# Kernel optimization log

Hardware: AMD Instinct MI355X
Metric: run time of the kernel (lower is better)

The kernel has to match this reference:

```python
import jax, jax.numpy as jnp
import numpy as np

BS = 16; N_PER = 1024; N = BS * N_PER; K = 9; E = N * K
H = 128; NODE_D = 64; EDGE_D = 16; RBF_DIM = 20; R_CUT = 1.0; L = 4; SF = 0.1


def setup_inputs():
    ks = jax.random.split(jax.random.key(0), 24)
    X = jax.random.normal(ks[0], (N, 3), dtype=jnp.float32) * 0.5
    node_attr = jax.random.normal(ks[1], (N, NODE_D), dtype=jnp.float32)
    edge_attr = jax.random.normal(ks[2], (E, EDGE_D), dtype=jnp.float32)
    idx = jnp.arange(N, dtype=jnp.int32)
    bid = idx // N_PER
    Seg = ((idx % N_PER) >= (N_PER // 2)).astype(jnp.int32)
    row = jnp.repeat(idx, K)
    col = (row // N_PER) * N_PER + jax.random.randint(ks[3], (E,), 0, N_PER, dtype=jnp.int32)
    edges = jnp.stack([row, col])

    def g(k, shape, fan):
        return jax.random.normal(k, shape, dtype=jnp.float32) * (1.0 / float(np.sqrt(fan)))

    MI = 2 * H + RBF_DIM + EDGE_D  # message MLP input dim
    return {
        'X': X, 'node_attr': node_attr, 'edge_attr': edge_attr,
        'W_in1': g(ks[4], (NODE_D, H), NODE_D), 'b_in1': jnp.zeros((H,), jnp.float32),
        'W_in2': g(ks[5], (H, H), H), 'b_in2': jnp.zeros((H,), jnp.float32),
        'We1': g(ks[6], (L, MI, H), MI), 'be1': jnp.zeros((L, H), jnp.float32),
        'We2': g(ks[7], (L, H, H), H), 'be2': jnp.zeros((L, H), jnp.float32),
        'Wv': g(ks[8], (L, H, H), H), 'Wvv': g(ks[9], (L, H, H), H),
        'Wh1': g(ks[10], (L, 2 * H, H), 2 * H), 'bh1': jnp.zeros((L, H), jnp.float32),
        'Wh2': g(ks[11], (L, H, H), H), 'bh2': jnp.zeros((L, H), jnp.float32),
        'Wi1': g(ks[12], (L, H, H), H), 'bi1': jnp.zeros((L, H), jnp.float32),
        'Wi2': g(ks[13], (L, H, H), H), 'bi2': jnp.zeros((L, H), jnp.float32),
        'Wgv1': g(ks[14], (H, H), H), 'Wgv2': g(ks[15], (H, H), H),
        'Wg1': g(ks[16], (2 * H, H), 2 * H), 'bg1': jnp.zeros((H,), jnp.float32),
        'Wg2': g(ks[17], (H, 2 * H), H), 'bg2': jnp.zeros((2 * H,), jnp.float32),
        'Wf': g(ks[18], (H, 9), H),
        'edges': edges, 'Seg': Seg, 'bid': bid,
    }


def _fwd(X, node_attr, edge_attr, W_in1, b_in1, W_in2, b_in2, We1, be1, We2, be2, Wv, Wvv, Wh1, bh1, Wh2, bh2, Wi1, bi1, Wi2, bi2, Wgv1, Wgv2, Wg1, bg1, Wg2, bg2, Wf, edges, Seg, bid):
    silu = jax.nn.silu
    row, col = edges[0], edges[1]
    nseg = 2 * BS
    seg_id = bid * 2 + Seg  # (complex, receptor/ligand) segment id
    # coord2radial + Bessel RBF with cosine cutoff
    diff = X[row] - X[col]
    norm = jnp.sqrt(jnp.sum(diff * diff, axis=-1)) + 1e-8
    unit = diff / norm[:, None]
    freqs = jnp.arange(1, RBF_DIM + 1, dtype=X.dtype) * (jnp.pi / R_CUT)
    rbf = jnp.sin(norm[:, None] * freqs[None, :]) / norm[:, None]
    cut = 0.5 * (jnp.cos(jnp.pi * jnp.clip(norm, 0.0, R_CUT) / R_CUT) + 1.0)
    rbf = rbf * cut[:, None]
    # in_conv
    h = silu(node_attr @ W_in1 + b_in1) @ W_in2 + b_in2
    v = jnp.zeros((N, H, 3), dtype=h.dtype)
    counts = jax.ops.segment_sum(jnp.ones((N,), dtype=h.dtype), seg_id, num_segments=nseg)
    opp = bid * 2 + (1 - Seg)  # opposite-molecule segment per node
    for i in range(L):
        # PINN message passing (PaiNN-style equivariant layer)
        m_in = jnp.concatenate([h[row], h[col], rbf, edge_attr], axis=-1)
        m = silu(m_in @ We1[i] + be1[i]) @ We2[i] + be2[i]  # [E, H]
        agg = jax.ops.segment_sum(m, row, num_segments=N)
        h_intra = h + silu(jnp.concatenate([h, agg], axis=-1) @ Wh1[i] + bh1[i]) @ Wh2[i] + bh2[i]
        v_msg = (m @ Wv[i])[:, :, None] * unit[:, None, :] + (m @ Wvv[i])[:, :, None] * v[col]
        v = v + jax.ops.segment_sum(v_msg, row, num_segments=N)
        # cross receptor<->ligand softmax attention: (H_a @ H_b.T).mean(1) == H_a @ mean(H_b)
        mean_h = jax.ops.segment_sum(h_intra, seg_id, num_segments=nseg) / counts[:, None]
        score = jnp.sum(h_intra * mean_h[opp], axis=-1)
        smax = jax.ops.segment_max(score, seg_id, num_segments=nseg)
        ex = jnp.exp(score - smax[seg_id])
        w = ex / jax.ops.segment_sum(ex, seg_id, num_segments=nseg)[seg_id]
        gated = h_intra * w[:, None]
        h = h_intra + silu(gated @ Wi1[i] + bi1[i]) @ Wi2[i] + bi2[i]
    # gated equivariant block
    v1 = jnp.einsum('nhc,hk->nkc', v, Wgv1)
    v2 = jnp.einsum('nhc,hk->nkc', v, Wgv2)
    v2n = jnp.sqrt(jnp.sum(v2 * v2, axis=-1) + 1e-8)
    mix = silu(jnp.concatenate([h, v2n], axis=-1) @ Wg1 + bg1) @ Wg2 + bg2
    h, bgate = mix[:, :H], mix[:, H:]
    v = v1 * bgate[:, :, None]
    # final_conv + per-(complex, molecule) pooled prediction vectors [2*BS, 9, 3]
    pv = jnp.einsum('nhc,ho->noc', v * h[:, :, None], Wf)
    pred = jax.ops.segment_sum(pv.reshape(N, 27), seg_id, num_segments=nseg).reshape(nseg, 9, 3)
    # kron/outer-product quadratic surface params: A [., 3, 3], b [., 3]
    A = (pred[:, 0, :, None] * pred[:, 1, None, :] + pred[:, 3, :, None] * pred[:, 2, None, :]
         + pred[:, 4, :, None] * pred[:, 5, None, :] + pred[:, 7, :, None] * pred[:, 6, None, :]) / (SF * SF)
    bvec = pred[:, 8] / SF
    return jnp.concatenate([A, bvec[:, :, None]], axis=2)  # [2*BS, 3, 4]


def reference(X, node_attr, edge_attr, W_in1, b_in1, W_in2, b_in2, We1, be1, We2, be2, Wv, Wvv, Wh1, bh1, Wh2, bh2, Wi1, bi1, Wi2, bi2, Wgv1, Wgv2, Wg1, bg1, Wg2, bg2, Wf, edges, Seg, bid):
    return _fwd(X, node_attr, edge_attr, W_in1, b_in1, W_in2, b_in2, We1, be1, We2, be2, Wv, Wvv, Wh1, bh1, Wh2, bh2, Wi1, bi1, Wi2, bi2, Wgv1, Wgv2, Wg1, bg1, Wg2, bg2, Wf, edges, Seg, bid)
```

## Files before the change

### kernel.cpp

```cpp
#include <hip/hip_runtime.h>
#include <math.h>

#define NN 16384
#define NE 147456
#define NSEGS 32
#define HD 128
#define RBF_D 20
#define EDGE_DD 16
#define NODE_DD 64
#define NLAYER 4
#define PI_F 3.14159265358979323846f


typedef __attribute__((ext_vector_type(8))) short v8s;
typedef __attribute__((ext_vector_type(4))) float v4f;
typedef __attribute__((ext_vector_type(8))) unsigned short v8u;

__device__ __forceinline__ unsigned short f2bf(float f) {
  union { float f; unsigned int u; } x; x.f = f;
  unsigned int u = x.u;
  return (unsigned short)((u + 0x7FFFu + ((u >> 16) & 1u)) >> 16);
}
__device__ __forceinline__ float bf2f(unsigned short b) {
  union { unsigned int u; float f; } x; x.u = ((unsigned int)b) << 16; return x.f;
}
__device__ __forceinline__ void split8(float4 a, float4 b, v8u& hi, v8u& lo) {
  float v[8] = {a.x, a.y, a.z, a.w, b.x, b.y, b.z, b.w};
#pragma unroll
  for (int i = 0; i < 8; i++) {
    unsigned short h = f2bf(v[i]);
    hi[i] = h;
    lo[i] = f2bf(v[i] - bf2f(h));
  }
}
__device__ __forceinline__ float silu_f(float v) { return v / (1.f + expf(-v)); }

struct WDesc { const float* src; const float* src2; unsigned short* hi; unsigned short* lo;
               int K; int N; int Kp; int ld; };
struct WDescs { WDesc d[48]; };
__global__ void wconv_k(WDescs ds) {
  WDesc d = ds.d[blockIdx.y];
  int idx = blockIdx.x * 256 + threadIdx.x;
  if (idx >= d.N * d.Kp) return;
  int n = idx / d.Kp, k = idx - n * d.Kp;
  const float* s = d.src; int nn = n;
  if (d.src2 && n >= 128) { s = d.src2; nn = n - 128; }
  float v = (k < d.K) ? s[(size_t)k * d.ld + nn] : 0.f;
  unsigned short h = f2bf(v);
  d.hi[idx] = h;
  d.lo[idx] = f2bf(v - bf2f(h));
}

__global__ void wcomb_k(const float* __restrict__ We2, const float* __restrict__ Wv,
                        const float* __restrict__ Wvv, float* __restrict__ Wc) {
  int l = blockIdx.z, which = blockIdx.y, xb = blockIdx.x;
  const float* A = We2 + (size_t)l * 128 * 128;
  const float* B = (which ? Wvv : Wv) + (size_t)l * 128 * 128;
  float* D = Wc + ((size_t)(which * NLAYER + l)) * 128 * 128;
  int n = threadIdx.x & 127, r2 = threadIdx.x >> 7;
#pragma unroll
  for (int i = 0; i < 8; i++) {
    int k1 = xb * 16 + r2 * 8 + i;
    float s = 0.f;
    for (int j = 0; j < 128; j++) s += A[k1 * 128 + j] * B[j * 128 + n];
    D[(size_t)k1 * 128 + n] = s;
  }
}
__global__ void bcomb_k(const float* __restrict__ be2, const float* __restrict__ Wv,
                        const float* __restrict__ Wvv, const float* __restrict__ be1,
                        float* __restrict__ bcv, float* __restrict__ bcvv,
                        float* __restrict__ b9, float* __restrict__ bx) {
  int l = blockIdx.x, n = threadIdx.x;
  const float* b = be2 + l * 128;
  float sv = 0.f, svv = 0.f;
  for (int j = 0; j < 128; j++) {
    sv  += b[j] * Wv[(size_t)l * 16384 + j * 128 + n];
    svv += b[j] * Wvv[(size_t)l * 16384 + j * 128 + n];
  }
  bcv[l * 128 + n] = sv; bcvv[l * 128 + n] = svv; b9[l * 128 + n] = 9.f * b[n];
  bx[l * 256 + n] = be1[l * 128 + n]; bx[l * 256 + 128 + n] = 0.f;
}

constexpr int LDS_S = 40;

template<int BM, int AMODE, int OUTM, int RESM>
__global__ __launch_bounds__(256, 2)
void mgemm_k(const float* A0f, const unsigned short* Ah0, const unsigned short* Al0,
             const unsigned short* __restrict__ Wth, const unsigned short* __restrict__ Wtl,
             int Kp, const float* __restrict__ bias, const float* __restrict__ resf,
             float* Cf, int ldc, unsigned short* Ch, unsigned short* Cl, int lda)
{
  constexpr int MT = BM / 32;
  __shared__ unsigned short Ah[BM * LDS_S], Al[BM * LDS_S];
  __shared__ unsigned short Bh[128 * LDS_S], Bl[128 * LDS_S];
  const int tid = threadIdx.x;
  const int m0 = blockIdx.x * BM;
  const int coff = blockIdx.y * 128;
  const int w = tid >> 6, lane = tid & 63;
  const int lm = lane & 15, kq = lane >> 4;
  const int wm = (w >> 1) * (BM / 2);
  const int wn = (w & 1) * 64;

  v4f acc[MT][4];
#pragma unroll
  for (int i = 0; i < MT; i++)
#pragma unroll
    for (int j = 0; j < 4; j++) acc[i][j] = (v4f){0.f, 0.f, 0.f, 0.f};

  const int KT = Kp >> 5;
  for (int kt = 0; kt < KT; kt++) {
#pragma unroll
    for (int i = 0; i < BM / 64; i++) {
      int m = i * 64 + (tid >> 2);
      int k8 = (tid & 3) * 8;
      int gk = kt * 32 + k8, gm = m0 + m;
      v8u hi, lo;
      if constexpr (AMODE == 1) {
        hi = *(const v8u*)&Ah0[(size_t)gm * 128 + gk];
        lo = *(const v8u*)&Al0[(size_t)gm * 128 + gk];
      } else {
        float4 a = *(const float4*)&A0f[(size_t)gm * lda + gk];
        float4 b = *(const float4*)&A0f[(size_t)gm * lda + gk + 4];
        split8(a, b, hi, lo);
      }
      *(v8u*)&Ah[m * LDS_S + k8] = hi;
      *(v8u*)&Al[m * LDS_S + k8] = lo;
    }
#pragma unroll
    for (int i = 0; i < 2; i++) {
      int f = i * 256 + tid;
      int n = f >> 2, k8 = (f & 3) * 8;
      size_t g = (size_t)(coff + n) * Kp + kt * 32 + k8;
      *(v8u*)&Bh[n * LDS_S + k8] = *(const v8u*)&Wth[g];
      *(v8u*)&Bl[n * LDS_S + k8] = *(const v8u*)&Wtl[g];
    }
    __syncthreads();
    v8s afh[MT], afl[MT];
#pragma unroll
    for (int mi = 0; mi < MT; mi++) {
      int r = wm + mi * 16 + lm;
      afh[mi] = *(v8s*)&Ah[r * LDS_S + kq * 8];
      afl[mi] = *(v8s*)&Al[r * LDS_S + kq * 8];
    }
#pragma unroll
    for (int ni = 0; ni < 4; ni++) {
      int r = wn + ni * 16 + lm;
      v8s bh = *(v8s*)&Bh[r * LDS_S + kq * 8];
      v8s bl = *(v8s*)&Bl[r * LDS_S + kq * 8];
#pragma unroll
      for (int mi = 0; mi < MT; mi++) {
        acc[mi][ni] = __builtin_amdgcn_mfma_f32_16x16x32_bf16(afh[mi], bh, acc[mi][ni], 0, 0, 0);
        acc[mi][ni] = __builtin_amdgcn_mfma_f32_16x16x32_bf16(afl[mi], bh, acc[mi][ni], 0, 0, 0);
        acc[mi][ni] = __builtin_amdgcn_mfma_f32_16x16x32_bf16(afh[mi], bl, acc[mi][ni], 0, 0, 0);
      }
    }
    __syncthreads();
  }
#pragma unroll
  for (int mi = 0; mi < MT; mi++) {
#pragma unroll
    for (int r = 0; r < 4; r++) {
      int mrow = m0 + wm + mi * 16 + kq * 4 + r;
#pragma unroll
      for (int ni = 0; ni < 4; ni++) {
        int ncol = coff + wn + ni * 16 + lm;
        float v = acc[mi][ni][r];
        if constexpr (RESM == 3) v += bias[ncol] * resf[mrow];
        else { if (bias) v += bias[ncol]; }
        if constexpr (OUTM == 0) Cf[(size_t)mrow * ldc + ncol] = v;
        else {
          unsigned short h = f2bf(v);
          Ch[(size_t)mrow * 128 + ncol] = h;
          Cl[(size_t)mrow * 128 + ncol] = f2bf(v - bf2f(h));
        }
      }
    }
  }
}

__device__ __forceinline__ float4 loadRE(const float* __restrict__ rbf,
                                         const float* __restrict__ ea, int m, int k4) {
  if (k4 < RBF_D) return *(const float4*)&rbf[(size_t)m * RBF_D + k4];
  if (k4 < RBF_D + EDGE_DD) return *(const float4*)&ea[(size_t)m * EDGE_DD + k4 - RBF_D];
  return make_float4(0.f, 0.f, 0.f, 0.f);
}

__global__ __launch_bounds__(256, 2)
void mre_k(const float* __restrict__ rbf, const float* __restrict__ ea,
           const float* __restrict__ hrc, const int* __restrict__ gcol,
           const unsigned short* __restrict__ Wth, const unsigned short* __restrict__ Wtl,
           unsigned short* __restrict__ m1h, unsigned short* __restrict__ m1l)
{
  constexpr int BM = 128, MT = 4, Kp = 64;
  __shared__ unsigned short Ah[BM * LDS_S], Al[BM * LDS_S];
  __shared__ unsigned short Bh[128 * LDS_S], Bl[128 * LDS_S];
  const int tid = threadIdx.x;
  const int m0 = blockIdx.x * BM;
  const int w = tid >> 6, lane = tid & 63;
  const int lm = lane & 15, kq = lane >> 4;
  const int wm = (w >> 1) * 64, wn = (w & 1) * 64;

  v4f acc[MT][4];
#pragma unroll
  for (int i = 0; i < MT; i++)
#pragma unroll
    for (int j = 0; j < 4; j++) acc[i][j] = (v4f){0.f, 0.f, 0.f, 0.f};

  for (int kt = 0; kt < Kp / 32; kt++) {
#pragma unroll
    for (int i = 0; i < 2; i++) {
      int m = i * 64 + (tid >> 2);
      int k8 = (tid & 3) * 8;
      int gk = kt * 32 + k8, gm = m0 + m;
      v8u hi, lo;
      split8(loadRE(rbf, ea, gm, gk), loadRE(rbf, ea, gm, gk + 4), hi, lo);
      *(v8u*)&Ah[m * LDS_S + k8] = hi;
      *(v8u*)&Al[m * LDS_S + k8] = lo;
    }
#pragma unroll
    for (int i = 0; i < 2; i++) {
      int f = i * 256 + tid;
      int n = f >> 2, k8 = (f & 3) * 8;
      size_t g = (size_t)n * Kp + kt * 32 + k8;
      *(v8u*)&Bh[n * LDS_S + k8] = *(const v8u*)&Wth[g];
      *(v8u*)&Bl[n * LDS_S + k8] = *(const v8u*)&Wtl[g];
    }
    __syncthreads();
    v8s afh[MT], afl[MT];
#pragma unroll
    for (int mi = 0; mi < MT; mi++) {
      int r = wm + mi * 16 + lm;
      afh[mi] = *(v8s*)&Ah[r * LDS_S + kq * 8];
      afl[mi] = *(v8s*)&Al[r * LDS_S + kq * 8];
    }
#pragma unroll
    for (int ni = 0; ni < 4; ni++) {
      int r = wn + ni * 16 + lm;
      v8s bh = *(v8s*)&Bh[r * LDS_S + kq * 8];
      v8s bl = *(v8s*)&Bl[r * LDS_S + kq * 8];
#pragma unroll
      for (int mi = 0; mi < MT; mi++) {
        acc[mi][ni] = __builtin_amdgcn_mfma_f32_16x16x32_bf16(afh[mi], bh, acc[mi][ni], 0, 0, 0);
        acc[mi][ni] = __builtin_amdgcn_mfma_f32_16x16x32_bf16(afl[mi], bh, acc[mi][ni], 0, 0, 0);
        acc[mi][ni] = __builtin_amdgcn_mfma_f32_16x16x32_bf16(afh[mi], bl, acc[mi][ni], 0, 0, 0);
      }
    }
    __syncthreads();
  }
#pragma unroll
  for (int mi = 0; mi < MT; mi++) {
#pragma unroll
    for (int r = 0; r < 4; r++) {
      int e = m0 + wm + mi * 16 + kq * 4 + r;
      int e9 = e / 9;
      int ce = gcol[e];
      const float* pr = hrc + (size_t)e9 * 256;
      const float* pc = hrc + (size_t)ce * 256 + 128;
#pragma unroll
      for (int ni = 0; ni < 4; ni++) {
        int nc = wn + ni * 16 + lm;
        float v = silu_f(acc[mi][ni][r] + pr[nc] + pc[nc]);
        unsigned short h = f2bf(v);
        m1h[(size_t)e * 128 + nc] = h;
        m1l[(size_t)e * 128 + nc] = f2bf(v - bf2f(h));
      }
    }
  }
}

template<int AMODE, int OUTM, int RESM>
__global__ __launch_bounds__(256, 2)
void mlp2_k(const float* A0f, const float* A1f,
            const unsigned short* Ah0, const unsigned short* Al0,
            const unsigned short* __restrict__ W1h, const unsigned short* __restrict__ W1l,
            int k1p, const float* __restrict__ b1,
            const unsigned short* __restrict__ W2h, const unsigned short* __restrict__ W2l,
            const float* __restrict__ b2,
            const float* resf, const unsigned short* resh, const unsigned short* resl,
            float* Cf, int ldc, unsigned short* Ch, unsigned short* Cl, int lda)
{
  __shared__ unsigned short Ah[64 * LDS_S], Al[64 * LDS_S];
  __shared__ unsigned short Bh[128 * LDS_S], Bl[128 * LDS_S];
  __shared__ unsigned short Th[64 * 136], Tl[64 * 136];
  const int tid = threadIdx.x;
  const int m0 = blockIdx.x * 64;
  const int w = tid >> 6, lane = tid & 63;
  const int lm = lane & 15, kq = lane >> 4;
  const int wm = (w >> 1) * 32, wn = (w & 1) * 64;

  v4f acc[2][4];
#pragma unroll
  for (int i = 0; i < 2; i++)
#pragma unroll
    for (int j = 0; j < 4; j++) acc[i][j] = (v4f){0.f, 0.f, 0.f, 0.f};

  for (int kt = 0; kt < (k1p >> 5); kt++) {
    {
      int m = tid >> 2, k8 = (tid & 3) * 8;
      int gk = kt * 32 + k8, gm = m0 + m;
      v8u hi, lo;
      if constexpr (AMODE == 3) {
        if (gk < 128) {
          hi = *(const v8u*)&Ah0[(size_t)gm * 128 + gk];
          lo = *(const v8u*)&Al0[(size_t)gm * 128 + gk];
        } else {
          float4 a = *(const float4*)&A1f[(size_t)gm * 128 + gk - 128];
          float4 b = *(const float4*)&A1f[(size_t)gm * 128 + gk - 124];
          split8(a, b, hi, lo);
        }
      } else {
        float4 a = *(const float4*)&A0f[(size_t)gm * lda + gk];
        float4 b = *(const float4*)&A0f[(size_t)gm * lda + gk + 4];
        if constexpr (AMODE == 4) {
          float s = A1f[gm];
          a.x *= s; a.y *= s; a.z *= s; a.w *= s;
          b.x *= s; b.y *= s; b.z *= s; b.w *= s;
        }
        split8(a, b, hi, lo);
      }
      *(v8u*)&Ah[m * LDS_S + k8] = hi;
      *(v8u*)&Al[m * LDS_S + k8] = lo;
    }
#pragma unroll
    for (int i = 0; i < 2; i++) {
      int f = i * 256 + tid;
      int n = f >> 2, k8 = (f & 3) * 8;
      size_t g = (size_t)n * k1p + kt * 32 + k8;
      *(v8u*)&Bh[n * LDS_S + k8] = *(const v8u*)&W1h[g];
      *(v8u*)&Bl[n * LDS_S + k8] = *(const v8u*)&W1l[g];
    }
    __syncthreads();
    v8s afh[2], afl[2];
#pragma unroll
    for (int mi = 0; mi < 2; mi++) {
      int r = wm + mi * 16 + lm;
      afh[mi] = *(v8s*)&Ah[r * LDS_S + kq * 8];
      afl[mi] = *(v8s*)&Al[r * LDS_S + kq * 8];
    }
#pragma unroll
    for (int ni = 0; ni < 4; ni++) {
      int r = wn + ni * 16 + lm;
      v8s bh = *(v8s*)&Bh[r * LDS_S + kq * 8];
      v8s bl = *(v8s*)&Bl[r * LDS_S + kq * 8];
#pragma unroll
      for (int mi = 0; mi < 2; mi++) {
        acc[mi][ni] = __builtin_amdgcn_mfma_f32_16x16x32_bf16(afh[mi], bh, acc[mi][ni], 0, 0, 0);
        acc[mi][ni] = __builtin_amdgcn_mfma_f32_16x16x32_bf16(afl[mi], bh, acc[mi][ni], 0, 0, 0);
        acc[mi][ni] = __builtin_amdgcn_mfma_f32_16x16x32_bf16(afh[mi], bl, acc[mi][ni], 0, 0, 0);
      }
    }
    __syncthreads();
  }
#pragma unroll
  for (int mi = 0; mi < 2; mi++) {
#pragma unroll
    for (int r = 0; r < 4; r++) {
      int row = wm + mi * 16 + kq * 4 + r;
#pragma unroll
      for (int ni = 0; ni < 4; ni++) {
        int col = wn + ni * 16 + lm;
        float v = silu_f(acc[mi][ni][r] + b1[col]);
        unsigned short h = f2bf(v);
        Th[row * 136 + col] = h;
        Tl[row * 136 + col] = f2bf(v - bf2f(h));
      }
    }
  }
  __syncthreads();
  const int coff2 = blockIdx.y * 128;
  v4f acc2[2][4];
#pragma unroll
  for (int i = 0; i < 2; i++)
#pragma unroll
    for (int j = 0; j < 4; j++) acc2[i][j] = (v4f){0.f, 0.f, 0.f, 0.f};
  for (int kt = 0; kt < 4; kt++) {
#pragma unroll
    for (int i = 0; i < 2; i++) {
      int f = i * 256 + tid;
      int n = f >> 2, k8 = (f & 3) * 8;
      size_t g = (size_t)(coff2 + n) * 128 + kt * 32 + k8;
      *(v8u*)&Bh[n * LDS_S + k8] = *(const v8u*)&W2h[g];
      *(v8u*)&Bl[n * LDS_S + k8] = *(const v8u*)&W2l[g];
    }
    __syncthreads();
    v8s afh[2], afl[2];
#pragma unroll
    for (int mi = 0; mi < 2; mi++) {
      int r = wm + mi * 16 + lm;
      afh[mi] = *(v8s*)&Th[r * 136 + kt * 32 + kq * 8];
      afl[mi] = *(v8s*)&Tl[r * 136 + kt * 32 + kq * 8];
    }
#pragma unroll
    for (int ni = 0; ni < 4; ni++) {
      int r = wn + ni * 16 + lm;
      v8s bh = *(v8s*)&Bh[r * LDS_S + kq * 8];
      v8s bl = *(v8s*)&Bl[r * LDS_S + kq * 8];
#pragma unroll
      for (int mi = 0; mi < 2; mi++) {
        acc2[mi][ni] = __builtin_amdgcn_mfma_f32_16x16x32_bf16(afh[mi], bh, acc2[mi][ni], 0, 0, 0);
        acc2[mi][ni] = __builtin_amdgcn_mfma_f32_16x16x32_bf16(afl[mi], bh, acc2[mi][ni], 0, 0, 0);
        acc2[mi][ni] = __builtin_amdgcn_mfma_f32_16x16x32_bf16(afh[mi], bl, acc2[mi][ni], 0, 0, 0);
      }
    }
    __syncthreads();
  }
#pragma unroll
  for (int mi = 0; mi < 2; mi++) {
#pragma unroll
    for (int r = 0; r < 4; r++) {
      int mrow = m0 + wm + mi * 16 + kq * 4 + r;
#pragma unroll
      for (int ni = 0; ni < 4; ni++) {
        int ncol = coff2 + wn + ni * 16 + lm;
        float v = acc2[mi][ni][r];
        if (b2) v += b2[ncol];
        if constexpr (RESM == 1) v += resf[(size_t)mrow * 128 + ncol];
        if constexpr (RESM == 2) v += bf2f(resh[(size_t)mrow * 128 + ncol]) + bf2f(resl[(size_t)mrow * 128 + ncol]);
        if constexpr (OUTM == 0) Cf[(size_t)mrow * ldc + ncol] = v;
        else {
          unsigned short h = f2bf(v);
          Ch[(size_t)mrow * 128 + ncol] = h;
          Cl[(size_t)mrow * 128 + ncol] = f2bf(v - bf2f(h));
        }
      }
    }
  }
}

__global__ void edge_geom_k(const float* __restrict__ X, const int* __restrict__ row,
                            const int* __restrict__ col,
                            float* __restrict__ unitv, float* __restrict__ rbf) {
  int e = blockIdx.x * 256 + threadIdx.x;
  if (e >= NE) return;
  int r = row[e], c = col[e];
  float dx = X[r * 3 + 0] - X[c * 3 + 0];
  float dy = X[r * 3 + 1] - X[c * 3 + 1];
  float dz = X[r * 3 + 2] - X[c * 3 + 2];
  float norm = sqrtf(dx * dx + dy * dy + dz * dz) + 1e-8f;
  float inv = 1.f / norm;
  unitv[e * 3 + 0] = dx * inv;
  unitv[e * 3 + 1] = dy * inv;
  unitv[e * 3 + 2] = dz * inv;
  float cl = fminf(norm, 1.0f);
  float cut = 0.5f * (cosf(PI_F * cl) + 1.0f);
  float s = cut * inv;
#pragma unroll
  for (int j = 0; j < RBF_D; j++) rbf[(size_t)e * RBF_D + j] = sinf(norm * (float)(j + 1) * PI_F) * s;
}

__global__ void sumU_k(const unsigned short* __restrict__ m1h, const unsigned short* __restrict__ m1l,
                       const float* __restrict__ unitv,
                       unsigned short* __restrict__ agh, unsigned short* __restrict__ agl,
                       float* __restrict__ U, float* __restrict__ sup) {
  int t = blockIdx.x * 256 + threadIdx.x;
  int n = t >> 7, hh = t & 127;
  float s = 0.f, u0 = 0.f, u1 = 0.f, u2 = 0.f;
#pragma unroll
  for (int k = 0; k < 9; k++) {
    int e = n * 9 + k;
    float m = bf2f(m1h[(size_t)e * 128 + hh]) + bf2f(m1l[(size_t)e * 128 + hh]);
    s += m;
    u0 += unitv[e * 3 + 0] * m;
    u1 += unitv[e * 3 + 1] * m;
    u2 += unitv[e * 3 + 2] * m;
  }
  unsigned short h = f2bf(s);
  agh[t] = h; agl[t] = f2bf(s - bf2f(h));
  U[(size_t)n * 128 + hh] = u0;
  U[(size_t)NN * 128 + (size_t)n * 128 + hh] = u1;
  U[(size_t)2 * NN * 128 + (size_t)n * 128 + hh] = u2;
  if (hh < 3) {
    float q = 0.f;
#pragma unroll
    for (int k = 0; k < 9; k++) q += unitv[(n * 9 + k) * 3 + hh];
    sup[hh * NN + n] = q;
  }
}

__global__ void vupd_k(const float* __restrict__ vold, const float* __restrict__ t1,
                       const unsigned short* __restrict__ mvvh, const unsigned short* __restrict__ mvvl,
                       const int* __restrict__ col, float* __restrict__ vnew) {
  const size_t P = (size_t)NN * 128;
  int t = blockIdx.x * 256 + threadIdx.x;
  int n = t >> 7, hh = t & 127;
  size_t b = (size_t)n * 128 + hh;
  float a0 = vold[b] + t1[b];
  float a1 = vold[P + b] + t1[P + b];
  float a2 = vold[2 * P + b] + t1[2 * P + b];
#pragma unroll
  for (int k = 0; k < 9; k++) {
    int e = n * 9 + k;
    int ce = col[e];
    float mvv = bf2f(mvvh[(size_t)e * 128 + hh]) + bf2f(mvvl[(size_t)e * 128 + hh]);
    size_t cb = (size_t)ce * 128 + hh;
    a0 += mvv * vold[cb];
    a1 += mvv * vold[P + cb];
    a2 += mvv * vold[2 * P + cb];
  }
  vnew[b] = a0; vnew[P + b] = a1; vnew[2 * P + b] = a2;
}

__global__ void meanh_k(const float* __restrict__ hintra, float* __restrict__ meanh) {
  __shared__ float red[512];
  int s = blockIdx.x, t = threadIdx.x;
  int c = t & 127, q = t >> 7;
  const float* p = hintra + (size_t)s * 512 * 128 + c;
  float a = 0.f;
  for (int i = q; i < 512; i += 4) a += p[(size_t)i * 128];
  red[t] = a;
  __syncthreads();
  if (q == 0) meanh[s * 128 + c] = (red[c] + red[128 + c] + red[256 + c] + red[384 + c]) * (1.f / 512.f);
}

__global__ void ssmax_k(const float* __restrict__ hintra, const float* __restrict__ meanh,
                        float* __restrict__ wgt) {
  __shared__ float mh[128];
  __shared__ float red[512];
  int s = blockIdx.x, t = threadIdx.x;
  if (t < 128) mh[t] = meanh[(s ^ 1) * 128 + t];
  __syncthreads();
  int n = s * 512 + t;
  const float* hp = hintra + (size_t)n * 128;
  float sc = 0.f;
  for (int h = 0; h < 128; h++) sc += hp[h] * mh[h];
  red[t] = sc;
  __syncthreads();
  for (int off = 256; off > 0; off >>= 1) {
    if (t < off) red[t] = fmaxf(red[t], red[t + off]);
    __syncthreads();
  }
  float mx = red[0];
  __syncthreads();
  float ex = expf(sc - mx);
  red[t] = ex;
  __syncthreads();
  for (int off = 256; off > 0; off >>= 1) {
    if (t < off) red[t] += red[t + off];
    __syncthreads();
  }
  wgt[n] = ex / red[0];
}

__global__ void v2n_k(const float* __restrict__ v12, float* __restrict__ v2n) {
  const size_t P = (size_t)NN * 256;
  int t = blockIdx.x * 256 + threadIdx.x;
  int n = t >> 7, h = t & 127;
  size_t b = (size_t)n * 256 + 128 + h;
  float a = v12[b], c = v12[P + b], d = v12[2 * P + b];
  v2n[t] = sqrtf(a * a + c * c + d * d + 1e-8f);
}

__global__ __launch_bounds__(256) void pv_k(const float* __restrict__ v12, const float* __restrict__ mix,
                     const float* __restrict__ Wf, float* __restrict__ pred) {
  __shared__ float red[4][28];
  const size_t P = (size_t)NN * 256;
  int t = threadIdx.x;
  int n = blockIdx.x * 256 + t;
  float acc[27];
#pragma unroll
  for (int j = 0; j < 27; j++) acc[j] = 0.f;
  const float* mxp = mix + (size_t)n * 256;
  const float* vp0 = v12 + (size_t)n * 256;
  const float* vp1 = vp0 + P;
  const float* vp2 = vp1 + P;
  for (int hh = 0; hh < HD; hh++) {
    float s = mxp[hh] * mxp[HD + hh];
    float sv0 = s * vp0[hh], sv1 = s * vp1[hh], sv2 = s * vp2[hh];
#pragma unroll
    for (int o = 0; o < 9; o++) {
      float wf = Wf[hh * 9 + o];
      acc[o * 3 + 0] += sv0 * wf;
      acc[o * 3 + 1] += sv1 * wf;
      acc[o * 3 + 2] += sv2 * wf;
    }
  }
#pragma unroll
  for (int j = 0; j < 27; j++) {
#pragma unroll
    for (int off = 32; off > 0; off >>= 1) acc[j] += __shfl_down(acc[j], off, 64);
  }
  int wave = t >> 6, lane = t & 63;
  if (lane == 0) {
#pragma unroll
    for (int j = 0; j < 27; j++) red[wave][j] = acc[j];
  }
  __syncthreads();
  if (t < 27) {
    float s = red[0][t] + red[1][t] + red[2][t] + red[3][t];
    atomicAdd(&pred[(blockIdx.x >> 1) * 27 + t], s);
  }
}

__global__ void out_k(const float* __restrict__ pred, float* __restrict__ out) {
  int s = threadIdx.x;
  if (s >= NSEGS) return;
  float p[27];
#pragma unroll
  for (int j = 0; j < 27; j++) p[j] = pred[s * 27 + j];
#pragma unroll
  for (int i = 0; i < 3; i++) {
#pragma unroll
    for (int j = 0; j < 3; j++) {
      float a = p[0 * 3 + i] * p[1 * 3 + j] + p[3 * 3 + i] * p[2 * 3 + j]
              + p[4 * 3 + i] * p[5 * 3 + j] + p[7 * 3 + i] * p[6 * 3 + j];
      out[s * 12 + i * 4 + j] = a * 100.f;
    }
    out[s * 12 + i * 4 + 3] = p[8 * 3 + i] * 10.f;
  }
}

extern "C" void kernel_launch(void* const* d_in, const int* in_sizes, int n_in,
                              void* d_out, int out_size, void* d_ws, size_t ws_size,
                              hipStream_t stream) {
  const float* X         = (const float*)d_in[0];
  const float* node_attr = (const float*)d_in[1];
  const float* edge_attr = (const float*)d_in[2];
  const float* W_in1 = (const float*)d_in[3];
  const float* b_in1 = (const float*)d_in[4];
  const float* W_in2 = (const float*)d_in[5];
  const float* b_in2 = (const float*)d_in[6];
  const float* We1 = (const float*)d_in[7];
  const float* be1 = (const float*)d_in[8];
  const float* We2 = (const float*)d_in[9];
  const float* be2 = (const float*)d_in[10];
  const float* Wv  = (const float*)d_in[11];
  const float* Wvv = (const float*)d_in[12];
  const float* Wh1 = (const float*)d_in[13];
  const float* bh1 = (const float*)d_in[14];
  const float* Wh2 = (const float*)d_in[15];
  const float* bh2 = (const float*)d_in[16];
  const float* Wi1 = (const float*)d_in[17];
  const float* bi1 = (const float*)d_in[18];
  const float* Wi2 = (const float*)d_in[19];
  const float* bi2 = (const float*)d_in[20];
  const float* Wgv1 = (const float*)d_in[21];
  const float* Wgv2 = (const float*)d_in[22];
  const float* Wg1 = (const float*)d_in[23];
  const float* bg1 = (const float*)d_in[24];
  const float* Wg2 = (const float*)d_in[25];
  const float* bg2 = (const float*)d_in[26];
  const float* Wf  = (const float*)d_in[27];
  const int* edges = (const int*)d_in[28];
  const int* rowp = edges;
  const int* colp = edges + NE;
  float* out = (float*)d_out;

  char* ws = (char*)d_ws;
  size_t o = 0;
  auto ab = [&](size_t bytes) { char* p = ws + o; o += (bytes + 255) & ~(size_t)255; return p; };
  float* unitv  = (float*)ab((size_t)NE * 3 * 4);
  float* rbf    = (float*)ab((size_t)NE * RBF_D * 4);
  float* va     = (float*)ab((size_t)NN * 384 * 4);
  float* vb     = (float*)ab((size_t)NN * 384 * 4);
  unsigned short* m1h = (unsigned short*)ab((size_t)NE * 128 * 2);
  unsigned short* m1l = (unsigned short*)ab((size_t)NE * 128 * 2);
  float* hrc    = (float*)ab((size_t)NN * 256 * 4);
  float* U      = (float*)ab((size_t)3 * NN * 128 * 4);
  float* sup    = (float*)ab((size_t)3 * NN * 4);
  float* agg    = (float*)ab((size_t)NN * 128 * 4);
  float* hintra = (float*)ab((size_t)NN * 128 * 4);
  unsigned short* agh = (unsigned short*)ab((size_t)NN * 128 * 2);
  unsigned short* agl = (unsigned short*)ab((size_t)NN * 128 * 2);
  unsigned short* hbh = (unsigned short*)ab((size_t)NN * 128 * 2);
  unsigned short* hbl = (unsigned short*)ab((size_t)NN * 128 * 2);
  float* meanh  = (float*)ab(NSEGS * 128 * 4);
  float* wgt    = (float*)ab(NN * 4);
  float* pred   = (float*)ab(NSEGS * 27 * 4);
  float* Wc     = (float*)ab((size_t)2 * NLAYER * 128 * 128 * 4);
  float* bcv    = (float*)ab(NLAYER * 128 * 4);
  float* bcvv   = (float*)ab(NLAYER * 128 * 4);
  float* b9     = (float*)ab(NLAYER * 128 * 4);
  float* bx     = (float*)ab(NLAYER * 256 * 4);
  unsigned short* wt = (unsigned short*)ab(4 * 1024 * 1024);
  float* v12  = (float*)m1l;
  float* mixb = (float*)m1h;

  size_t wo = 0;
  auto walloc = [&](size_t n) { unsigned short* p = wt + wo; wo += n; return p; };
  WDescs wd{};
  int wcnt = 0;
  auto addw = [&](const float* src, const float* src2, int K, int N, int Kp, int ld) {
    size_t sz = (size_t)N * Kp;
    unsigned short* hi = walloc(sz);
    unsigned short* lo = walloc(sz);
    wd.d[wcnt] = WDesc{src, src2, hi, lo, K, N, Kp, ld};
    return wcnt++;
  };
  int iWin1 = addw(W_in1, nullptr, 64, 128, 64, 128);
  int iWin2 = addw(W_in2, nullptr, 128, 128, 128, 128);
  int iWe1rc[NLAYER], iWe1re[NLAYER], iWe2[NLAYER], iWcv[NLAYER], iWcvv[NLAYER],
      iWh1[NLAYER], iWh2[NLAYER], iWi1[NLAYER], iWi2[NLAYER];
  for (int i = 0; i < NLAYER; i++) {
    const float* Wl = We1 + (size_t)i * 292 * 128;
    iWe1rc[i] = addw(Wl, Wl + 128 * 128, 128, 256, 128, 128);
    iWe1re[i] = addw(Wl + 256 * 128, nullptr, 36, 128, 64, 128);
    iWe2[i]   = addw(We2 + (size_t)i * 16384, nullptr, 128, 128, 128, 128);
    iWcv[i]   = addw(Wc + (size_t)i * 16384, nullptr, 128, 128, 128, 128);
    iWcvv[i]  = addw(Wc + (size_t)(NLAYER + i) * 16384, nullptr, 128, 128, 128, 128);
    iWh1[i]   = addw(Wh1 + (size_t)i * 256 * 128, nullptr, 256, 128, 256, 128);
    iWh2[i]   = addw(Wh2 + (size_t)i * 16384, nullptr, 128, 128, 128, 128);
    iWi1[i]   = addw(Wi1 + (size_t)i * 16384, nullptr, 128, 128, 128, 128);
    iWi2[i]   = addw(Wi2 + (size_t)i * 16384, nullptr, 128, 128, 128, 128);
  }
  int iWg1   = addw(Wg1, nullptr, 256, 128, 256, 128);
  int iWg2   = addw(Wg2, nullptr, 128, 256, 128, 256);
  int iWgv12 = addw(Wgv1, Wgv2, 128, 256, 128, 128);

  hipMemsetAsync(va, 0, (size_t)NN * 384 * sizeof(float), stream);
  hipMemsetAsync(pred, 0, NSEGS * 27 * sizeof(float), stream);

  wcomb_k<<<dim3(8, 2, NLAYER), 256, 0, stream>>>(We2, Wv, Wvv, Wc);
  bcomb_k<<<NLAYER, 128, 0, stream>>>(be2, Wv, Wvv, be1, bcv, bcvv, b9, bx);
  wconv_k<<<dim3(128, wcnt), 256, 0, stream>>>(wd);
  edge_geom_k<<<NE / 256, 256, 0, stream>>>(X, rowp, colp, unitv, rbf);

  auto WH = [&](int idx) { return wd.d[idx].hi; };
  auto WL = [&](int idx) { return wd.d[idx].lo; };

  mlp2_k<0, 1, 0><<<dim3(NN / 64, 1), 256, 0, stream>>>(
      node_attr, nullptr, nullptr, nullptr,
      WH(iWin1), WL(iWin1), 64, b_in1, WH(iWin2), WL(iWin2), b_in2,
      nullptr, nullptr, nullptr, nullptr, 128, hbh, hbl, NODE_DD);

  float* vcur = va;
  float* vnxt = vb;
  for (int i = 0; i < NLAYER; i++) {
    mgemm_k<64, 1, 0, 0><<<dim3(NN / 64, 2), 256, 0, stream>>>(
        nullptr, hbh, hbl, WH(iWe1rc[i]), WL(iWe1rc[i]), 128,
        bx + i * 256, nullptr, hrc, 256, nullptr, nullptr, 0);
    mre_k<<<NE / 128, 256, 0, stream>>>(rbf, edge_attr, hrc, colp,
        WH(iWe1re[i]), WL(iWe1re[i]), m1h, m1l);
    sumU_k<<<NN * 128 / 256, 256, 0, stream>>>(m1h, m1l, unitv, agh, agl, U, sup);
    mgemm_k<64, 1, 0, 0><<<dim3(NN / 64, 1), 256, 0, stream>>>(
        nullptr, agh, agl, WH(iWe2[i]), WL(iWe2[i]), 128,
        b9 + i * 128, nullptr, agg, 128, nullptr, nullptr, 0);
    mlp2_k<3, 0, 2><<<dim3(NN / 64, 1), 256, 0, stream>>>(
        nullptr, agg, hbh, hbl,
        WH(iWh1[i]), WL(iWh1[i]), 256, bh1 + i * 128, WH(iWh2[i]), WL(iWh2[i]), bh2 + i * 128,
        nullptr, hbh, hbl, hintra, 128, nullptr, nullptr, 0);
    meanh_k<<<NSEGS, 512, 0, stream>>>(hintra, meanh);
    ssmax_k<<<NSEGS, 512, 0, stream>>>(hintra, meanh, wgt);
    mgemm_k<64, 0, 0, 3><<<dim3(3 * NN / 64, 1), 256, 0, stream>>>(
        U, nullptr, nullptr, WH(iWcv[i]), WL(iWcv[i]), 128,
        bcv + i * 128, sup, U, 128, nullptr, nullptr, 128);
    mgemm_k<128, 1, 1, 0><<<dim3(NE / 128, 1), 256, 0, stream>>>(
        nullptr, m1h, m1l, WH(iWcvv[i]), WL(iWcvv[i]), 128,
        bcvv + i * 128, nullptr, nullptr, 128, m1h, m1l, 0);
    vupd_k<<<NN * 128 / 256, 256, 0, stream>>>(vcur, U, m1h, m1l, colp, vnxt);
    { float* t = vcur; vcur = vnxt; vnxt = t; }
    mlp2_k<4, 1, 1><<<dim3(NN / 64, 1), 256, 0, stream>>>(
        hintra, wgt, nullptr, nullptr,
        WH(iWi1[i]), WL(iWi1[i]), 128, bi1 + i * 128, WH(iWi2[i]), WL(iWi2[i]), bi2 + i * 128,
        hintra, nullptr, nullptr, nullptr, 128, hbh, hbl, 128);
  }

  mgemm_k<64, 0, 0, 0><<<dim3(3 * NN / 64, 2), 256, 0, stream>>>(
      vcur, nullptr, nullptr, WH(iWgv12), WL(iWgv12), 128,
      nullptr, nullptr, v12, 256, nullptr, nullptr, 128);
  v2n_k<<<NN * 128 / 256, 256, 0, stream>>>(v12, agg);
  mlp2_k<3, 0, 0><<<dim3(NN / 64, 2), 256, 0, stream>>>(
      nullptr, agg, hbh, hbl,
      WH(iWg1), WL(iWg1), 256, bg1, WH(iWg2), WL(iWg2), bg2,
      nullptr, nullptr, nullptr, mixb, 256, nullptr, nullptr, 0);
  pv_k<<<NN / 256, 256, 0, stream>>>(v12, mixb, Wf, pred);
  out_k<<<1, 64, 0, stream>>>(pred, out);
}
```

Measured before the change: 1.336 ms.

## Fuse segment mean and softmax kernels, widen sumU loads, re-parallelize pooling

Merges meanh_k and ssmax_k into one attnp_k launch, where each 1024-thread block handles a segment pair and computes both means in shared memory. sumU_k now processes two channels per thread with ushort2/float2 vector loads and stores. pv_k is restructured from 64 blocks, each thread walking a full node row with 27 accumulators, to 2048 blocks of 8 nodes, with a gate product staged in shared memory and one output component per thread. This removes one launch per layer and raises parallelism in the final pooling, at the cost of more atomics and redundant Wf and v12 reads in pv_k.

```diff
diff --git a/kernel.cpp b/kernel.cpp
--- a/kernel.cpp
+++ b/kernel.cpp
@@ -453,27 +453,35 @@
                        unsigned short* __restrict__ agh, unsigned short* __restrict__ agl,
                        float* __restrict__ U, float* __restrict__ sup) {
   int t = blockIdx.x * 256 + threadIdx.x;
-  int n = t >> 7, hh = t & 127;
-  float s = 0.f, u0 = 0.f, u1 = 0.f, u2 = 0.f;
+  int n = t >> 6, p = t & 63;
+  int h2 = p * 2;
+  float s0 = 0, s1 = 0, u00 = 0, u01 = 0, u10 = 0, u11 = 0, u20 = 0, u21 = 0;
 #pragma unroll
   for (int k = 0; k < 9; k++) {
     int e = n * 9 + k;
-    float m = bf2f(m1h[(size_t)e * 128 + hh]) + bf2f(m1l[(size_t)e * 128 + hh]);
-    s += m;
-    u0 += unitv[e * 3 + 0] * m;
-    u1 += unitv[e * 3 + 1] * m;
-    u2 += unitv[e * 3 + 2] * m;
-  }
-  unsigned short h = f2bf(s);
-  agh[t] = h; agl[t] = f2bf(s - bf2f(h));
-  U[(size_t)n * 128 + hh] = u0;
-  U[(size_t)NN * 128 + (size_t)n * 128 + hh] = u1;
-  U[(size_t)2 * NN * 128 + (size_t)n * 128 + hh] = u2;
-  if (hh < 3) {
+    ushort2 mh = *(const ushort2*)&m1h[(size_t)e * 128 + h2];
+    ushort2 ml = *(const ushort2*)&m1l[(size_t)e * 128 + h2];
+    float m0 = bf2f(mh.x) + bf2f(ml.x);
+    float m1 = bf2f(mh.y) + bf2f(ml.y);
+    float u0 = unitv[e * 3 + 0], u1 = unitv[e * 3 + 1], u2 = unitv[e * 3 + 2];
+    s0 += m0; s1 += m1;
+    u00 += u0 * m0; u01 += u0 * m1;
+    u10 += u1 * m0; u11 += u1 * m1;
+    u20 += u2 * m0; u21 += u2 * m1;
+  }
+  unsigned short h0 = f2bf(s0), h1 = f2bf(s1);
+  size_t b = (size_t)n * 128 + h2;
+  *(ushort2*)&agh[b] = make_ushort2(h0, h1);
+  *(ushort2*)&agl[b] = make_ushort2(f2bf(s0 - bf2f(h0)), f2bf(s1 - bf2f(h1)));
+  const size_t P = (size_t)NN * 128;
+  *(float2*)&U[b]         = make_float2(u00, u01);
+  *(float2*)&U[P + b]     = make_float2(u10, u11);
+  *(float2*)&U[2 * P + b] = make_float2(u20, u21);
+  if (p < 3) {
     float q = 0.f;
 #pragma unroll
-    for (int k = 0; k < 9; k++) q += unitv[(n * 9 + k) * 3 + hh];
-    sup[hh * NN + n] = q;
+    for (int k = 0; k < 9; k++) q += unitv[(n * 9 + k) * 3 + p];
+    sup[p * NN + n] = q;
   }
 }
 
@@ -500,45 +508,49 @@
   vnew[b] = a0; vnew[P + b] = a1; vnew[2 * P + b] = a2;
 }
 
-__global__ void meanh_k(const float* __restrict__ hintra, float* __restrict__ meanh) {
-  __shared__ float red[512];
-  int s = blockIdx.x, t = threadIdx.x;
-  int c = t & 127, q = t >> 7;
-  const float* p = hintra + (size_t)s * 512 * 128 + c;
-  float a = 0.f;
-  for (int i = q; i < 512; i += 4) a += p[(size_t)i * 128];
-  red[t] = a;
+__global__ __launch_bounds__(1024)
+void attnp_k(const float* __restrict__ hintra, float* __restrict__ wgt) {
+  __shared__ float red[1024];
+  __shared__ float mhs[256];
+  int t = threadIdx.x;
+  int base = blockIdx.x * 1024;
+  {
+    int q = t >> 7, c = t & 127;
+    int a = q >> 2, qq = q & 3;
+    const float* p = hintra + (size_t)(base + a * 512) * 128 + c;
+    float s = 0.f;
+    for (int r = qq; r < 512; r += 4) s += p[(size_t)r * 128];
+    red[t] = s;
+  }
   __syncthreads();
-  if (q == 0) meanh[s * 128 + c] = (red[c] + red[128 + c] + red[256 + c] + red[384 + c]) * (1.f / 512.f);
-}
-
-__global__ void ssmax_k(const float* __restrict__ hintra, const float* __restrict__ meanh,
-                        float* __restrict__ wgt) {
-  __shared__ float mh[128];
-  __shared__ float red[512];
-  int s = blockIdx.x, t = threadIdx.x;
-  if (t < 128) mh[t] = meanh[(s ^ 1) * 128 + t];
+  if (t < 256) {
+    int aa = t >> 7, cc = t & 127;
+    float m = (red[(aa * 4 + 0) * 128 + cc] + red[(aa * 4 + 1) * 128 + cc] +
+               red[(aa * 4 + 2) * 128 + cc] + red[(aa * 4 + 3) * 128 + cc]) * (1.f / 512.f);
+    mhs[aa * 128 + cc] = m;
+  }
   __syncthreads();
-  int n = s * 512 + t;
-  const float* hp = hintra + (size_t)n * 128;
+  int ha = t >> 9;
+  const float* mh = mhs + (1 - ha) * 128;
+  const float* hp = hintra + (size_t)(base + t) * 128;
   float sc = 0.f;
   for (int h = 0; h < 128; h++) sc += hp[h] * mh[h];
   red[t] = sc;
   __syncthreads();
   for (int off = 256; off > 0; off >>= 1) {
-    if (t < off) red[t] = fmaxf(red[t], red[t + off]);
-    __syncthreads();
-  }
-  float mx = red[0];
+    if ((t & 511) < off) red[t] = fmaxf(red[t], red[t + off]);
+    __syncthreads();
+  }
+  float mx = red[ha << 9];
   __syncthreads();
   float ex = expf(sc - mx);
   red[t] = ex;
   __syncthreads();
   for (int off = 256; off > 0; off >>= 1) {
-    if (t < off) red[t] += red[t + off];
-    __syncthreads();
-  }
-  wgt[n] = ex / red[0];
+    if ((t & 511) < off) red[t] += red[t + off];
+    __syncthreads();
+  }
+  wgt[base + t] = ex / red[ha << 9];
 }
 
 __global__ void v2n_k(const float* __restrict__ v12, float* __restrict__ v2n) {
@@ -550,44 +562,35 @@
   v2n[t] = sqrtf(a * a + c * c + d * d + 1e-8f);
 }
 
-__global__ __launch_bounds__(256) void pv_k(const float* __restrict__ v12, const float* __restrict__ mix,
-                     const float* __restrict__ Wf, float* __restrict__ pred) {
-  __shared__ float red[4][28];
+__global__ __launch_bounds__(256)
+void pv_k(const float* __restrict__ v12, const float* __restrict__ mix,
+          const float* __restrict__ Wf, float* __restrict__ pred) {
+  __shared__ float sg[8][128];
+  __shared__ float pr[8][32];
   const size_t P = (size_t)NN * 256;
   int t = threadIdx.x;
-  int n = blockIdx.x * 256 + t;
-  float acc[27];
-#pragma unroll
-  for (int j = 0; j < 27; j++) acc[j] = 0.f;
-  const float* mxp = mix + (size_t)n * 256;
-  const float* vp0 = v12 + (size_t)n * 256;
-  const float* vp1 = vp0 + P;
-  const float* vp2 = vp1 + P;
-  for (int hh = 0; hh < HD; hh++) {
-    float s = mxp[hh] * mxp[HD + hh];
-    float sv0 = s * vp0[hh], sv1 = s * vp1[hh], sv2 = s * vp2[hh];
-#pragma unroll
-    for (int o = 0; o < 9; o++) {
-      float wf = Wf[hh * 9 + o];
-      acc[o * 3 + 0] += sv0 * wf;
-      acc[o * 3 + 1] += sv1 * wf;
-      acc[o * 3 + 2] += sv2 * wf;
-    }
-  }
-#pragma unroll
-  for (int j = 0; j < 27; j++) {
-#pragma unroll
-    for (int off = 32; off > 0; off >>= 1) acc[j] += __shfl_down(acc[j], off, 64);
-  }
-  int wave = t >> 6, lane = t & 63;
-  if (lane == 0) {
-#pragma unroll
-    for (int j = 0; j < 27; j++) red[wave][j] = acc[j];
+  int nb = blockIdx.x * 8;
+#pragma unroll
+  for (int i = 0; i < 4; i++) {
+    int idx = i * 256 + t;
+    int nn = idx >> 7, hh = idx & 127;
+    const float* mxp = mix + (size_t)(nb + nn) * 256;
+    sg[nn][hh] = mxp[hh] * mxp[128 + hh];
   }
   __syncthreads();
-  if (t < 27) {
-    float s = red[0][t] + red[1][t] + red[2][t] + red[3][t];
-    atomicAdd(&pred[(blockIdx.x >> 1) * 27 + t], s);
+  int nn = t >> 5, j = t & 31;
+  float acc = 0.f;
+  if (j < 27) {
+    int o = j / 3, c = j - o * 3;
+    const float* vp = v12 + (size_t)c * P + (size_t)(nb + nn) * 256;
+    for (int hh = 0; hh < 128; hh++) acc += sg[nn][hh] * vp[hh] * Wf[hh * 9 + o];
+  }
+  pr[nn][j] = acc;
+  __syncthreads();
+  if (t < 32) {
+    float s = pr[0][t] + pr[1][t] + pr[2][t] + pr[3][t] +
+              pr[4][t] + pr[5][t] + pr[6][t] + pr[7][t];
+    if (t < 27) atomicAdd(&pred[(nb >> 9) * 27 + t], s);
   }
 }
 
@@ -663,7 +666,6 @@
   unsigned short* agl = (unsigned short*)ab((size_t)NN * 128 * 2);
   unsigned short* hbh = (unsigned short*)ab((size_t)NN * 128 * 2);
   unsigned short* hbl = (unsigned short*)ab((size_t)NN * 128 * 2);
-  float* meanh  = (float*)ab(NSEGS * 128 * 4);
   float* wgt    = (float*)ab(NN * 4);
   float* pred   = (float*)ab(NSEGS * 27 * 4);
   float* Wc     = (float*)ab((size_t)2 * NLAYER * 128 * 128 * 4);
@@ -730,7 +732,7 @@
         bx + i * 256, nullptr, hrc, 256, nullptr, nullptr, 0);
     mre_k<<<NE / 128, 256, 0, stream>>>(rbf, edge_attr, hrc, colp,
         WH(iWe1re[i]), WL(iWe1re[i]), m1h, m1l);
-    sumU_k<<<NN * 128 / 256, 256, 0, stream>>>(m1h, m1l, unitv, agh, agl, U, sup);
+    sumU_k<<<NN * 64 / 256, 256, 0, stream>>>(m1h, m1l, unitv, agh, agl, U, sup);
     mgemm_k<64, 1, 0, 0><<<dim3(NN / 64, 1), 256, 0, stream>>>(
         nullptr, agh, agl, WH(iWe2[i]), WL(iWe2[i]), 128,
         b9 + i * 128, nullptr, agg, 128, nullptr, nullptr, 0);
@@ -738,8 +740,7 @@
         nullptr, agg, hbh, hbl,
         WH(iWh1[i]), WL(iWh1[i]), 256, bh1 + i * 128, WH(iWh2[i]), WL(iWh2[i]), bh2 + i * 128,
         nullptr, hbh, hbl, hintra, 128, nullptr, nullptr, 0);
-    meanh_k<<<NSEGS, 512, 0, stream>>>(hintra, meanh);
-    ssmax_k<<<NSEGS, 512, 0, stream>>>(hintra, meanh, wgt);
+    attnp_k<<<16, 1024, 0, stream>>>(hintra, wgt);
     mgemm_k<64, 0, 0, 3><<<dim3(3 * NN / 64, 1), 256, 0, stream>>>(
         U, nullptr, nullptr, WH(iWcv[i]), WL(iWcv[i]), 128,
         bcv + i * 128, sup, U, 128, nullptr, nullptr, 128);
@@ -762,6 +763,6 @@
       nullptr, agg, hbh, hbl,
       WH(iWg1), WL(iWg1), 256, bg1, WH(iWg2), WL(iWg2), bg2,
       nullptr, nullptr, nullptr, mixb, 256, nullptr, nullptr, 0);
-  pv_k<<<NN / 256, 256, 0, stream>>>(v12, mixb, Wf, pred);
+  pv_k<<<NN / 8, 256, 0, stream>>>(v12, mixb, Wf, pred);
   out_k<<<1, 64, 0, stream>>>(pred, out);
 }
```

Measured after the change: 1.337 ms. Within noise of the previous version (+0.1%).
